# Kernel tuning notes

Measured on AMD Instinct MI355X. Metric: run time of the kernel, lower is better.

## Reference

```python
import jax, jax.numpy as jnp
import numpy as np

B = 1; H = 192; W = 192; DIM = 128; HEADS = 8
WS = 16                      # window_size
OWS = 24                     # overlap_win_size = int(16*0.5)+16
PAD = 4                      # (OWS-WS)//2
C2 = DIM // 2                # per-branch channels
H2 = HEADS // 2              # per-branch heads
HID = 256                    # mlp_ratio * dim
TBL = (WS + OWS - 1) ** 2    # 1521 rel-pos table entries
SCALE = (C2 // H2) ** (-0.5) # head_dim ** -0.5


def layer_norm(x, w, b, eps=1e-5):
    mu = jnp.mean(x, -1, keepdims=True)
    var = jnp.mean((x - mu) ** 2, -1, keepdims=True)
    return (x - mu) * jax.lax.rsqrt(var + eps) * w + b


def window_partition(x, ws):
    b, h, w, c = x.shape
    x = x.reshape(b, h // ws, ws, w // ws, ws, c).transpose(0, 1, 3, 2, 4, 5)
    return x.reshape(-1, ws, ws, c)


def window_reverse(win, ws, h, w):
    b = win.shape[0] // ((h // ws) * (w // ws))
    x = win.reshape(b, h // ws, w // ws, ws, ws, -1).transpose(0, 1, 3, 2, 4, 5)
    return x.reshape(b, h, w, -1)


def _patch_idx(h, w):
    ri = (jnp.arange(h // WS) * WS)[:, None] + jnp.arange(OWS)  # (nwh, OWS)
    ci = (jnp.arange(w // WS) * WS)[:, None] + jnp.arange(OWS)  # (nww, OWS)
    return ri, ci


def unfold_patches(x):
    # x: (b, h, w, c) -> (b*nw, OWS*OWS, c); matches nn.Unfold(OWS, stride=WS, pad=PAD)
    b, h, w, c = x.shape
    xp = jnp.pad(x, ((0, 0), (PAD, PAD), (PAD, PAD), (0, 0)))
    ri, ci = _patch_idx(h, w)
    p = xp[:, ri[:, None, :, None], ci[None, :, None, :], :]  # (b,nwh,nww,OWS,OWS,c)
    return p.reshape(-1, OWS * OWS, c)


def fold_patches(p, b, h, w):
    # inverse of unfold: scatter-add overlapping patches into (b, h+2PAD, w+2PAD, c)
    nwh, nww = h // WS, w // WS
    c = p.shape[-1]
    p = p.reshape(b, nwh, nww, OWS, OWS, c)
    ri, ci = _patch_idx(h, w)
    canvas = jnp.zeros((b, h + 2 * PAD, w + 2 * PAD, c), p.dtype)
    return canvas.at[:, ri[:, None, :, None], ci[None, :, None, :], :].add(p)


def cubic_kernel(x, A=-0.75):
    # PyTorch bicubic (cubic convolution, A=-0.75)
    ax = jnp.abs(x)
    w1 = ((A + 2.0) * ax - (A + 3.0)) * ax * ax + 1.0
    w2 = A * (ax * (ax * (ax - 5.0) + 8.0) - 4.0)
    return jnp.where(ax <= 1.0, w1, jnp.where(ax < 2.0, w2, 0.0))


def resize_matrix(n_out, n_in):
    # dense 1-D bicubic resize matrix, align_corners=False, border-clamped (torch semantics)
    i = jnp.arange(n_out, dtype=jnp.float32)
    src = (i + 0.5) * (float(n_in) / float(n_out)) - 0.5
    fl = jnp.floor(src)
    idx = fl[:, None] + jnp.arange(-1, 3, dtype=jnp.float32)[None, :]  # (n_out, 4)
    wts = cubic_kernel(src[:, None] - idx)
    idx_c = jnp.clip(idx, 0, n_in - 1).astype(jnp.int32)
    M = jnp.zeros((n_out, n_in), jnp.float32)
    return M.at[jnp.arange(n_out)[:, None], idx_c].add(wts)


def cross_attn(xq, xkv, rpi, wq, wkv, rpb):
    b_, nq, d = xq.shape
    n = xkv.shape[1]
    q = (xq @ wq).reshape(b_, nq, H2, -1).transpose(0, 2, 1, 3)
    k, v = jnp.split(xkv @ wkv, 2, axis=-1)
    k = k.reshape(b_, n, H2, -1).transpose(0, 2, 1, 3)
    v = v.reshape(b_, n, H2, -1).transpose(0, 2, 1, 3)
    attn = jnp.einsum('bhqd,bhkd->bhqk', q * SCALE, k)
    bias = rpb[rpi.reshape(-1)].reshape(WS * WS, OWS * OWS, H2)
    bias = bias.transpose(2, 0, 1) if nq < n else bias.transpose(2, 1, 0)
    attn = jax.nn.softmax(attn + bias[None], axis=-1)
    out = jnp.einsum('bhqk,bhkd->bhqd', attn, v)
    return out.transpose(0, 2, 1, 3).reshape(b_, nq, d)


def gsfn(x, h, w, fc1_w, fc1_b, sgn_w, sgn_b, conv_w, conv_b, fc2_w, fc2_b):
    x = x @ fc1_w + fc1_b  # NOTE: source GSFN never applies self.act
    x1, x2 = jnp.split(x, 2, axis=-1)
    Bn, N, Ch = x2.shape
    x2 = layer_norm(x2, sgn_w, sgn_b).transpose(0, 2, 1).reshape(Bn, Ch, h, w)
    x2 = jax.lax.conv_general_dilated(
        x2, conv_w, (1, 1), ((1, 1), (1, 1)),
        feature_group_count=Ch, dimension_numbers=('NCHW', 'OIHW', 'NCHW'))
    x2 = x2 + conv_b[None, :, None, None]
    x2 = x2.reshape(Bn, Ch, N).transpose(0, 2, 1)
    return (x1 * x2) @ fc2_w + fc2_b


def mstb(x_tkn, ln1_w, ln1_b, q1_w, kv1_w, rpb1, q2_w, kv2_w, rpb2,
         proj_w, proj_b, ln2_w, ln2_b, fc1_w, fc1_b, sgn_w, sgn_b,
         conv_w, conv_b, fc2_w, fc2_b, rpi, h, w):
    b, _, c = x_tkn.shape
    short = x_tkn
    x = layer_norm(x_tkn, ln1_w, ln1_b).reshape(b, h, w, c)
    xw = window_partition(x, WS).reshape(-1, WS * WS, c)     # (b*nw, ws*ws, c)
    xa, xb = jnp.split(xw, 2, axis=-1)
    xb_img = window_reverse(xb.reshape(-1, WS, WS, C2), WS, h, w)  # (b,h,w,C2)
    xb_p = unfold_patches(xb_img)                            # (b*nw, OWS*OWS, C2)
    a = cross_attn(xa, xb_p, rpi, q1_w, kv1_w, rpb1) + xa
    bb = cross_attn(xb_p, xa, rpi, q2_w, kv2_w, rpb2) + xb_p
    folded = fold_patches(bb, b, h, w)                       # (b, h+2p, w+2p, C2)
    Mh = resize_matrix(h, h + 2 * PAD)
    Mw = resize_matrix(w, w + 2 * PAD)
    resized = jnp.einsum('oi,bijc,pj->bopc', Mh, folded, Mw)  # bicubic to (h,w)
    xb2 = window_partition(resized, WS).reshape(-1, WS * WS, C2)
    x = jnp.concatenate([a, xb2], -1)
    x = window_reverse(x.reshape(-1, WS, WS, c), WS, h, w).reshape(b, h * w, c)
    x = x @ proj_w + proj_b + short
    x = gsfn(layer_norm(x, ln2_w, ln2_b), h, w, fc1_w, fc1_b,
             sgn_w, sgn_b, conv_w, conv_b, fc2_w, fc2_b) + x
    return x


def setup_inputs() -> dict:
    key = jax.random.key(0)
    ks = jax.random.split(key, 12)
    rn = lambda k, s, sc: jax.random.normal(k, s, jnp.float32) * sc
    return {
        'x_tkn': jax.random.normal(ks[0], (B, H * W, DIM), jnp.float32),
        'ln1_w': jnp.ones((DIM,), jnp.float32), 'ln1_b': jnp.zeros((DIM,), jnp.float32),
        'q1_w': rn(ks[1], (C2, C2), 0.05), 'kv1_w': rn(ks[2], (C2, 2 * C2), 0.05),
        'rpb1': rn(ks[3], (TBL, H2), 0.02),
        'q2_w': rn(ks[4], (C2, C2), 0.05), 'kv2_w': rn(ks[5], (C2, 2 * C2), 0.05),
        'rpb2': rn(ks[6], (TBL, H2), 0.02),
        'proj_w': rn(ks[7], (DIM, DIM), 0.05), 'proj_b': jnp.zeros((DIM,), jnp.float32),
        'ln2_w': jnp.ones((DIM,), jnp.float32), 'ln2_b': jnp.zeros((DIM,), jnp.float32),
        'fc1_w': rn(ks[8], (DIM, HID), 0.05), 'fc1_b': jnp.zeros((HID,), jnp.float32),
        'sgn_w': jnp.ones((HID // 2,), jnp.float32), 'sgn_b': jnp.zeros((HID // 2,), jnp.float32),
        'conv_w': rn(ks[9], (HID // 2, 1, 3, 3), 0.1), 'conv_b': jnp.zeros((HID // 2,), jnp.float32),
        'fc2_w': rn(ks[10], (HID // 2, DIM), 0.05), 'fc2_b': jnp.zeros((DIM,), jnp.float32),
        'rpi': jax.random.randint(ks[11], (WS * WS, OWS * OWS), 0, TBL),
        'h': H, 'w': W,
    }


def reference(x_tkn, ln1_w, ln1_b, q1_w, kv1_w, rpb1, q2_w, kv2_w, rpb2,
              proj_w, proj_b, ln2_w, ln2_b, fc1_w, fc1_b, sgn_w, sgn_b,
              conv_w, conv_b, fc2_w, fc2_b, rpi, h, w):
    return mstb(x_tkn, ln1_w, ln1_b, q1_w, kv1_w, rpb1, q2_w, kv2_w, rpb2,
                proj_w, proj_b, ln2_w, ln2_b, fc1_w, fc1_b, sgn_w, sgn_b,
                conv_w, conv_b, fc2_w, fc2_b, rpi, h, w)
```

## Files before the change

kernel.cpp:

```cpp
#include <hip/hip_runtime.h>
#include <hip/hip_bf16.h>

#define HH 192
#define WW 192
#define NWIN 12
#define WSZ 16
#define OWSZ 24
#define PADK 4
#define NQ1 256
#define NKV1 576
#define C2K 64
#define H2K 4
#define HD 16
#define NTOK (HH*WW)
#define LOG2E 1.4426950408889634f
#define QSCALE (0.25f * LOG2E)

typedef __hip_bfloat16 bf16;
typedef __attribute__((ext_vector_type(8))) short bf16x8;
typedef __attribute__((ext_vector_type(4))) float f32x4;

union B8 { short s[8]; bf16x8 v; unsigned u[4]; };

__device__ __forceinline__ unsigned cvtpk(float lo, float hi)
{
    unsigned r;
    asm("v_cvt_pk_bf16_f32 %0, %1, %2" : "=v"(r) : "v"(lo), "v"(hi));
    return r;
}

__launch_bounds__(256)
__global__ void ln_kernel(const float* __restrict__ in, int is, int io,
                          float* __restrict__ out, int os, int oo,
                          const float* __restrict__ g, const float* __restrict__ b,
                          int M)
{
    int row = blockIdx.x * 4 + (threadIdx.x >> 6);
    if (row >= M) return;
    int lane = threadIdx.x & 63;
    const float* p = in + (size_t)row * is + io;
    float v0 = p[lane * 2], v1 = p[lane * 2 + 1];
    float s = v0 + v1, sq = v0 * v0 + v1 * v1;
#pragma unroll
    for (int o = 32; o > 0; o >>= 1) { s += __shfl_xor(s, o); sq += __shfl_xor(sq, o); }
    float mu  = s * 0.0078125f;
    float var = sq * 0.0078125f - mu * mu;
    float inv = 1.0f / sqrtf(var + 1e-5f);
    float* q = out + (size_t)row * os + oo;
    q[lane * 2]     = (v0 - mu) * inv * g[lane * 2]     + b[lane * 2];
    q[lane * 2 + 1] = (v1 - mu) * inv * g[lane * 2 + 1] + b[lane * 2 + 1];
}

__global__ void wcomb_kernel(const float* __restrict__ q1_w, const float* __restrict__ kv1_w,
                             const float* __restrict__ q2_w, const float* __restrict__ kv2_w,
                             float* __restrict__ W)
{
    int idx = blockIdx.x * 256 + threadIdx.x;
    if (idx >= 128 * 384) return;
    int r = idx / 384, c = idx % 384;
    float v = 0.f;
    if (c < 64)       { if (r < 64)  v = q1_w[r * 64 + c]; }
    else if (c < 192) { if (r >= 64) v = kv1_w[(r - 64) * 128 + (c - 64)]; }
    else if (c < 256) { if (r >= 64) v = q2_w[(r - 64) * 64 + (c - 192)]; }
    else              { if (r < 64)  v = kv2_w[r * 128 + (c - 256)]; }
    W[idx] = v;
}

__global__ void bias1_kernel(const float* __restrict__ rpb1, const int* __restrict__ rpi,
                             float* __restrict__ biasT)
{
    int idx = blockIdx.x * 256 + threadIdx.x;
    if (idx >= H2K * NKV1 * NQ1) return;
    int q = idx & 255;
    int n = (idx >> 8) % NKV1;
    int h = idx / (NKV1 * NQ1);
    biasT[idx] = rpb1[rpi[q * NKV1 + n] * H2K + h] * LOG2E;
}

__global__ void bias2_kernel(const float* __restrict__ rpb2, const int* __restrict__ rpi,
                             float* __restrict__ biasT)
{
    int idx = blockIdx.x * 256 + threadIdx.x;
    if (idx >= H2K * NQ1 * NKV1) return;
    int q = idx % NKV1;
    int k = (idx / NKV1) % NQ1;
    int h = idx / (NKV1 * NQ1);
    biasT[idx] = rpb2[rpi[k * NKV1 + q] * H2K + h] * LOG2E;
}

__launch_bounds__(256)
__global__ void attn1_mfma(const float* __restrict__ qkvA,
                           const float* __restrict__ lnx,
                           const float* __restrict__ biasT,
                           float* __restrict__ xcat)
{
    __shared__ unsigned K_lds[NKV1][12];
    __shared__ unsigned V_lds[NKV1][12];

    const int win = blockIdx.x, h = blockIdx.y;
    const int wi = win / NWIN, wj = win % NWIN;
    const int tid = threadIdx.x;
    const int lane = tid & 63, w = tid >> 6;
    const int g = lane >> 4, qloc = lane & 15;

    for (int n = tid; n < NKV1; n += 256) {
        int rr = wi * WSZ - PADK + n / OWSZ, cc = wj * WSZ - PADK + n % OWSZ;
        bool ib = (rr >= 0 && rr < HH && cc >= 0 && cc < WW);
        unsigned kw[8], vw[8];
        if (ib) {
            const float* kp = qkvA + (size_t)(rr * WW + cc) * 192 + 64 + h * HD;
#pragma unroll
            for (int u = 0; u < 8; u++) {
                kw[u] = cvtpk(kp[2 * u], kp[2 * u + 1]);
                vw[u] = cvtpk(kp[64 + 2 * u], kp[64 + 2 * u + 1]);
            }
        } else {
#pragma unroll
            for (int u = 0; u < 8; u++) { kw[u] = 0; vw[u] = 0; }
        }
        *(uint4*)&K_lds[n][0] = make_uint4(kw[0], kw[1], kw[2], kw[3]);
        *(uint4*)&K_lds[n][4] = make_uint4(kw[4], kw[5], kw[6], kw[7]);
        *(uint4*)&V_lds[n][0] = make_uint4(vw[0], vw[1], vw[2], vw[3]);
        *(uint4*)&V_lds[n][4] = make_uint4(vw[4], vw[5], vw[6], vw[7]);
    }
    __syncthreads();

    const int q0base = blockIdx.z * 128 + w * 32;
    bf16x8 qfrag[2];
#pragma unroll
    for (int qt = 0; qt < 2; qt++) {
        int q = q0base + qt * 16 + qloc;
        int pix = (wi * WSZ + (q >> 4)) * WW + wj * WSZ + (q & 15);
        B8 f;
#pragma unroll
        for (int j = 0; j < 4; j++) f.u[j] = 0;
        if (g < 2) {
            const float* qp = qkvA + (size_t)pix * 192 + h * HD + 8 * g;
#pragma unroll
            for (int j = 0; j < 4; j++)
                f.u[j] = cvtpk(qp[2 * j] * QSCALE, qp[2 * j + 1] * QSCALE);
        }
        qfrag[qt] = f.v;
    }

    f32x4 O[2];
    float lsum[2];
#pragma unroll
    for (int qt = 0; qt < 2; qt++) { O[qt] = (f32x4){0.f, 0.f, 0.f, 0.f}; lsum[qt] = 0.f; }
    const f32x4 zz = {0.f, 0.f, 0.f, 0.f};

    for (int step = 0; step < 18; step++) {
        const int k0 = step * 32;
        bf16x8 kfA, kfB;
        if (g < 2) {
            kfA = *(const bf16x8*)&K_lds[k0 + qloc][4 * g];
            kfB = *(const bf16x8*)&K_lds[k0 + 16 + qloc][4 * g];
        } else {
            B8 zf;
#pragma unroll
            for (int j = 0; j < 4; j++) zf.u[j] = 0;
            kfA = zf.v; kfB = zf.v;
        }
        B8 vf;
#pragma unroll
        for (int j = 0; j < 8; j++) {
            int key = k0 + 4 * g + (j & 3) + ((j >> 2) << 4);
            unsigned word = V_lds[key][qloc >> 1];
            vf.s[j] = (short)((qloc & 1) ? (word >> 16) : (word & 0xffff));
        }

#pragma unroll
        for (int qt = 0; qt < 2; qt++) {
            f32x4 sA = __builtin_amdgcn_mfma_f32_16x16x32_bf16(kfA, qfrag[qt], zz, 0, 0, 0);
            f32x4 sB = __builtin_amdgcn_mfma_f32_16x16x32_bf16(kfB, qfrag[qt], zz, 0, 0, 0);
            int qa = q0base + qt * 16 + qloc;
            const float* bpA = biasT + ((size_t)h * NKV1 + k0 + 4 * g) * NQ1 + qa;
            const float* bpB = bpA + 16 * NQ1;
            float pa[4], pb[4];
            float ls = 0.f;
#pragma unroll
            for (int r = 0; r < 4; r++) {
                pa[r] = exp2f(sA[r] + bpA[(size_t)r * NQ1]);
                pb[r] = exp2f(sB[r] + bpB[(size_t)r * NQ1]);
                ls += pa[r] + pb[r];
            }
            B8 pf;
            pf.u[0] = cvtpk(pa[0], pa[1]);
            pf.u[1] = cvtpk(pa[2], pa[3]);
            pf.u[2] = cvtpk(pb[0], pb[1]);
            pf.u[3] = cvtpk(pb[2], pb[3]);
            lsum[qt] += ls;
            O[qt] = __builtin_amdgcn_mfma_f32_16x16x32_bf16(vf.v, pf.v, O[qt], 0, 0, 0);
        }
    }

#pragma unroll
    for (int qt = 0; qt < 2; qt++) {
        float lt = lsum[qt];
        lt += __shfl_xor(lt, 16);
        lt += __shfl_xor(lt, 32);
        float rl = 1.f / lt;
        int q = q0base + qt * 16 + qloc;
        int pix = (wi * WSZ + (q >> 4)) * WW + wj * WSZ + (q & 15);
        size_t base = (size_t)pix * 128 + h * HD + 4 * g;
#pragma unroll
        for (int r = 0; r < 4; r++)
            xcat[base + r] = O[qt][r] * rl + lnx[base + r];
    }
}

__launch_bounds__(256)
__global__ void attn2_mfma(const float* __restrict__ qkvB,
                           const float* __restrict__ lnx,
                           const float* __restrict__ biasT,
                           float* __restrict__ bb)
{
    __shared__ unsigned K_lds[NQ1][12];
    __shared__ unsigned V_lds[NQ1][12];

    const int win = blockIdx.x, h = blockIdx.y;
    const int wi = win / NWIN, wj = win % NWIN;
    const int tid = threadIdx.x;
    const int lane = tid & 63, w = tid >> 6;
    const int g = lane >> 4, qloc = lane & 15;

    if (tid < NQ1) {
        int n = tid;
        int pix = (wi * WSZ + (n >> 4)) * WW + wj * WSZ + (n & 15);
        const float* kp = qkvB + (size_t)pix * 192 + 64 + h * HD;
        unsigned kw[8], vw[8];
#pragma unroll
        for (int u = 0; u < 8; u++) {
            kw[u] = cvtpk(kp[2 * u], kp[2 * u + 1]);
            vw[u] = cvtpk(kp[64 + 2 * u], kp[64 + 2 * u + 1]);
        }
        *(uint4*)&K_lds[n][0] = make_uint4(kw[0], kw[1], kw[2], kw[3]);
        *(uint4*)&K_lds[n][4] = make_uint4(kw[4], kw[5], kw[6], kw[7]);
        *(uint4*)&V_lds[n][0] = make_uint4(vw[0], vw[1], vw[2], vw[3]);
        *(uint4*)&V_lds[n][4] = make_uint4(vw[4], vw[5], vw[6], vw[7]);
    }
    __syncthreads();

    const int q0base = blockIdx.z * 192 + w * 48;
    bf16x8 qfrag[3];
    bool qin[3];
    int qpix[3];
#pragma unroll
    for (int qt = 0; qt < 3; qt++) {
        int qa = q0base + qt * 16 + qloc;
        int gr = wi * WSZ - PADK + qa / OWSZ, gc = wj * WSZ - PADK + qa % OWSZ;
        bool ib = (gr >= 0 && gr < HH && gc >= 0 && gc < WW);
        qin[qt] = ib;
        qpix[qt] = ib ? gr * WW + gc : 0;
        B8 f;
#pragma unroll
        for (int j = 0; j < 4; j++) f.u[j] = 0;
        if (ib && g < 2) {
            const float* qp = qkvB + (size_t)qpix[qt] * 192 + h * HD + 8 * g;
#pragma unroll
            for (int j = 0; j < 4; j++)
                f.u[j] = cvtpk(qp[2 * j] * QSCALE, qp[2 * j + 1] * QSCALE);
        }
        qfrag[qt] = f.v;
    }

    f32x4 O[3];
    float lsum[3];
#pragma unroll
    for (int qt = 0; qt < 3; qt++) { O[qt] = (f32x4){0.f, 0.f, 0.f, 0.f}; lsum[qt] = 0.f; }
    const f32x4 zz = {0.f, 0.f, 0.f, 0.f};

    for (int step = 0; step < 8; step++) {
        const int k0 = step * 32;
        bf16x8 kfA, kfB;
        if (g < 2) {
            kfA = *(const bf16x8*)&K_lds[k0 + qloc][4 * g];
            kfB = *(const bf16x8*)&K_lds[k0 + 16 + qloc][4 * g];
        } else {
            B8 zf;
#pragma unroll
            for (int j = 0; j < 4; j++) zf.u[j] = 0;
            kfA = zf.v; kfB = zf.v;
        }
        B8 vf;
#pragma unroll
        for (int j = 0; j < 8; j++) {
            int key = k0 + 4 * g + (j & 3) + ((j >> 2) << 4);
            unsigned word = V_lds[key][qloc >> 1];
            vf.s[j] = (short)((qloc & 1) ? (word >> 16) : (word & 0xffff));
        }

#pragma unroll
        for (int qt = 0; qt < 3; qt++) {
            f32x4 sA = __builtin_amdgcn_mfma_f32_16x16x32_bf16(kfA, qfrag[qt], zz, 0, 0, 0);
            f32x4 sB = __builtin_amdgcn_mfma_f32_16x16x32_bf16(kfB, qfrag[qt], zz, 0, 0, 0);
            int qa = q0base + qt * 16 + qloc;
            const float* bpA = biasT + ((size_t)h * NQ1 + k0 + 4 * g) * NKV1 + qa;
            const float* bpB = bpA + 16 * NKV1;
            float pa[4], pb[4];
            float ls = 0.f;
#pragma unroll
            for (int r = 0; r < 4; r++) {
                pa[r] = exp2f(sA[r] + bpA[(size_t)r * NKV1]);
                pb[r] = exp2f(sB[r] + bpB[(size_t)r * NKV1]);
                ls += pa[r] + pb[r];
            }
            B8 pf;
            pf.u[0] = cvtpk(pa[0], pa[1]);
            pf.u[1] = cvtpk(pa[2], pa[3]);
            pf.u[2] = cvtpk(pb[0], pb[1]);
            pf.u[3] = cvtpk(pb[2], pb[3]);
            lsum[qt] += ls;
            O[qt] = __builtin_amdgcn_mfma_f32_16x16x32_bf16(vf.v, pf.v, O[qt], 0, 0, 0);
        }
    }

#pragma unroll
    for (int qt = 0; qt < 3; qt++) {
        float lt = lsum[qt];
        lt += __shfl_xor(lt, 16);
        lt += __shfl_xor(lt, 32);
        float rl = 1.f / lt;
        int qa = q0base + qt * 16 + qloc;
        size_t obase = ((size_t)win * NKV1 + qa) * C2K + h * HD + 4 * g;
        size_t rbase = (size_t)qpix[qt] * 128 + C2K + h * HD + 4 * g;
#pragma unroll
        for (int r = 0; r < 4; r++)
            bb[obase + r] = O[qt][r] * rl + (qin[qt] ? lnx[rbase + r] : 0.f);
    }
}

__global__ void fold_kernel(const float* __restrict__ bb, float* __restrict__ folded)
{
    int idx = blockIdx.x * 256 + threadIdx.x;
    if (idx >= 200 * 200 * 64) return;
    int c = idx & 63;
    int j = (idx >> 6) % 200;
    int i = idx / (64 * 200);
    int ilo = (i > 23) ? ((i - 8) >> 4) : 0;
    int ihi = min(11, i >> 4);
    int jlo = (j > 23) ? ((j - 8) >> 4) : 0;
    int jhi = min(11, j >> 4);
    float s = 0.f;
    for (int wi = ilo; wi <= ihi; wi++)
        for (int wj = jlo; wj <= jhi; wj++) {
            int p = (i - wi * 16) * OWSZ + (j - wj * 16);
            s += bb[((size_t)(wi * NWIN + wj) * NKV1 + p) * C2K + c];
        }
    folded[idx] = s;
}

__device__ __forceinline__ float cubicw(float x)
{
    float ax = fabsf(x);
    const float A = -0.75f;
    if (ax <= 1.f) return ((A + 2.f) * ax - (A + 3.f)) * ax * ax + 1.f;
    if (ax < 2.f)  return A * (ax * (ax * (ax - 5.f) + 8.f) - 4.f);
    return 0.f;
}

__global__ void resize_kernel(const float* __restrict__ folded, float* __restrict__ xcat)
{
    int idx = blockIdx.x * 256 + threadIdx.x;
    if (idx >= HH * WW * C2K) return;
    int c = idx & 63;
    int p = (idx >> 6) % WW;
    int o = idx / (C2K * WW);
    const float ratio = 200.f / 192.f;
    float sr = (o + 0.5f) * ratio - 0.5f;
    float sc = (p + 0.5f) * ratio - 0.5f;
    int fr = (int)floorf(sr), fcc = (int)floorf(sc);
    float wc[4]; int ic[4];
#pragma unroll
    for (int u = 0; u < 4; u++) {
        int jj = fcc - 1 + u;
        wc[u] = cubicw(sc - (float)jj);
        ic[u] = min(max(jj, 0), 199);
    }
    float acc = 0.f;
#pragma unroll
    for (int t = 0; t < 4; t++) {
        int ii = fr - 1 + t;
        float wr = cubicw(sr - (float)ii);
        int ir = min(max(ii, 0), 199);
        const float* rowp = folded + ((size_t)ir * 200) * 64 + c;
        float rs = 0.f;
#pragma unroll
        for (int u = 0; u < 4; u++) rs += wc[u] * rowp[(size_t)ic[u] * 64];
        acc += wr * rs;
    }
    xcat[(size_t)(o * WW + p) * 128 + C2K + c] = acc;
}

template<int NTPW>
__launch_bounds__(256)
__global__ void gemm_mfma(const float* __restrict__ A1, int a1s,
                          const float* __restrict__ A2, int a2s,
                          const float* __restrict__ Wm, int ldb,
                          const float* __restrict__ bias,
                          const float* __restrict__ R, int rs,
                          float* __restrict__ C, int cs)
{
    const int tid = threadIdx.x;
    const int lane = tid & 63, w = tid >> 6;
    const int g = lane >> 4, nl = lane & 15;

    bf16x8 wf[NTPW][4];
#pragma unroll
    for (int t = 0; t < NTPW; t++) {
        int ncol = (w * NTPW + t) * 16 + nl;
#pragma unroll
        for (int ks = 0; ks < 4; ks++) {
            const float* wp = Wm + (size_t)(ks * 32 + 8 * g) * ldb + ncol;
            B8 f;
#pragma unroll
            for (int j = 0; j < 4; j++)
                f.u[j] = cvtpk(wp[(size_t)(2 * j) * ldb], wp[(size_t)(2 * j + 1) * ldb]);
            wf[t][ks] = f.v;
        }
    }

    const f32x4 zz = {0.f, 0.f, 0.f, 0.f};
    for (int it = 0; it < 4; it++) {
        const int row = (blockIdx.x * 4 + it) * 16 + nl;
        bf16x8 xf[4];
        const float* ap = A1 + (size_t)row * a1s + 8 * g;
#pragma unroll
        for (int ks = 0; ks < 4; ks++) {
            float4 v0 = *(const float4*)(ap + ks * 32);
            float4 v1 = *(const float4*)(ap + ks * 32 + 4);
            if (A2) {
                const float* ap2 = A2 + (size_t)row * a2s + 8 * g + ks * 32;
                float4 m0 = *(const float4*)(ap2);
                float4 m1 = *(const float4*)(ap2 + 4);
                v0.x *= m0.x; v0.y *= m0.y; v0.z *= m0.z; v0.w *= m0.w;
                v1.x *= m1.x; v1.y *= m1.y; v1.z *= m1.z; v1.w *= m1.w;
            }
            B8 f;
            f.u[0] = cvtpk(v0.x, v0.y);
            f.u[1] = cvtpk(v0.z, v0.w);
            f.u[2] = cvtpk(v1.x, v1.y);
            f.u[3] = cvtpk(v1.z, v1.w);
            xf[ks] = f.v;
        }

        f32x4 acc[NTPW];
#pragma unroll
        for (int t = 0; t < NTPW; t++) acc[t] = zz;
#pragma unroll
        for (int ks = 0; ks < 4; ks++)
#pragma unroll
            for (int t = 0; t < NTPW; t++)
                acc[t] = __builtin_amdgcn_mfma_f32_16x16x32_bf16(wf[t][ks], xf[ks], acc[t], 0, 0, 0);

#pragma unroll
        for (int t = 0; t < NTPW; t++) {
            const int n0t = (w * NTPW + t) * 16 + 4 * g;
            float4 o;
            o.x = acc[t][0]; o.y = acc[t][1]; o.z = acc[t][2]; o.w = acc[t][3];
            if (bias) {
                float4 bv = *(const float4*)(bias + n0t);
                o.x += bv.x; o.y += bv.y; o.z += bv.z; o.w += bv.w;
            }
            if (R) {
                float4 rv = *(const float4*)(R + (size_t)row * rs + n0t);
                o.x += rv.x; o.y += rv.y; o.z += rv.z; o.w += rv.w;
            }
            *(float4*)(C + (size_t)row * cs + n0t) = o;
        }
    }
}

__global__ void dwconv_kernel(const float* __restrict__ x2n,
                              const float* __restrict__ conv_w,
                              const float* __restrict__ conv_b,
                              float* __restrict__ x2c)
{
    int idx = blockIdx.x * 256 + threadIdx.x;
    if (idx >= NTOK * 128) return;
    int ch = idx & 127, t = idx >> 7;
    int i = t / WW, j = t % WW;
    float acc = conv_b[ch];
#pragma unroll
    for (int a = 0; a < 3; a++) {
        int ii = i + a - 1;
        if (ii < 0 || ii >= HH) continue;
#pragma unroll
        for (int b = 0; b < 3; b++) {
            int jj = j + b - 1;
            if (jj < 0 || jj >= WW) continue;
            acc += conv_w[ch * 9 + a * 3 + b] * x2n[(size_t)(ii * WW + jj) * 256 + ch];
        }
    }
    x2c[(size_t)t * 128 + ch] = acc;
}

extern "C" void kernel_launch(void* const* d_in, const int* in_sizes, int n_in,
                              void* d_out, int out_size, void* d_ws, size_t ws_size,
                              hipStream_t stream)
{
    (void)in_sizes; (void)n_in; (void)out_size; (void)ws_size;
    const float* x_tkn  = (const float*)d_in[0];
    const float* ln1_w  = (const float*)d_in[1];
    const float* ln1_b  = (const float*)d_in[2];
    const float* q1_w   = (const float*)d_in[3];
    const float* kv1_w  = (const float*)d_in[4];
    const float* rpb1   = (const float*)d_in[5];
    const float* q2_w   = (const float*)d_in[6];
    const float* kv2_w  = (const float*)d_in[7];
    const float* rpb2   = (const float*)d_in[8];
    const float* proj_w = (const float*)d_in[9];
    const float* proj_b = (const float*)d_in[10];
    const float* ln2_w  = (const float*)d_in[11];
    const float* ln2_b  = (const float*)d_in[12];
    const float* fc1_w  = (const float*)d_in[13];
    const float* fc1_b  = (const float*)d_in[14];
    const float* sgn_w  = (const float*)d_in[15];
    const float* sgn_b  = (const float*)d_in[16];
    const float* conv_w = (const float*)d_in[17];
    const float* conv_b = (const float*)d_in[18];
    const float* fc2_w  = (const float*)d_in[19];
    const float* fc2_b  = (const float*)d_in[20];
    const int*   rpi    = (const int*)d_in[21];

    float* ws = (float*)d_ws;
    float* lnx    = ws;
    float* xcat   = ws + 4718592;
    float* bbuf   = ws + 9437184;
    float* bias1T = ws + 14745600;
    float* bias2T = ws + 17104896;
    float* wcomb  = ws + 17694720;
    float* qkv    = ws + 17743872;
    float* foldp  = ws + 17743872;
    float* h1     = ws + 14745600;
    float* out    = (float*)d_out;

    ln_kernel<<<NTOK / 4, 256, 0, stream>>>(x_tkn, 128, 0, lnx, 128, 0, ln1_w, ln1_b, NTOK);
    wcomb_kernel<<<(128 * 384 + 255) / 256, 256, 0, stream>>>(q1_w, kv1_w, q2_w, kv2_w, wcomb);
    bias1_kernel<<<(H2K * NKV1 * NQ1) / 256, 256, 0, stream>>>(rpb1, rpi, bias1T);
    bias2_kernel<<<(H2K * NQ1 * NKV1) / 256, 256, 0, stream>>>(rpb2, rpi, bias2T);
    gemm_mfma<3><<<NTOK / 64, 256, 0, stream>>>(lnx, 128, nullptr, 0, wcomb, 384,
                                                nullptr, nullptr, 0, qkv, 192);
    attn1_mfma<<<dim3(144, 4, 2), 256, 0, stream>>>(qkv, lnx, bias1T, xcat);
    gemm_mfma<3><<<NTOK / 64, 256, 0, stream>>>(lnx, 128, nullptr, 0, wcomb + 192, 384,
                                                nullptr, nullptr, 0, qkv, 192);
    attn2_mfma<<<dim3(144, 4, 3), 256, 0, stream>>>(qkv, lnx, bias2T, bbuf);
    fold_kernel<<<(200 * 200 * 64) / 256, 256, 0, stream>>>(bbuf, foldp);
    resize_kernel<<<(HH * WW * C2K) / 256, 256, 0, stream>>>(foldp, xcat);
    gemm_mfma<2><<<NTOK / 64, 256, 0, stream>>>(xcat, 128, nullptr, 0, proj_w, 128,
                                                proj_b, x_tkn, 128, lnx, 128);
    ln_kernel<<<NTOK / 4, 256, 0, stream>>>(lnx, 128, 0, bbuf, 128, 0, ln2_w, ln2_b, NTOK);
    gemm_mfma<4><<<NTOK / 64, 256, 0, stream>>>(bbuf, 128, nullptr, 0, fc1_w, 256,
                                                fc1_b, nullptr, 0, h1, 256);
    ln_kernel<<<NTOK / 4, 256, 0, stream>>>(h1, 256, 128, h1, 256, 128, sgn_w, sgn_b, NTOK);
    dwconv_kernel<<<(NTOK * 128) / 256, 256, 0, stream>>>(h1 + 128, conv_w, conv_b, xcat);
    gemm_mfma<2><<<NTOK / 64, 256, 0, stream>>>(h1, 256, xcat, 128, fc2_w, 128,
                                                fc2_b, lnx, 128, out, 128);
}
```

Baseline: 320.3 us.

## Store QKV in bf16, pre-transpose bf16 weights, and split GEMM rows across grid

The QKV GEMMs now write bf16 output with the attention scale folded into the Q weights, so the attention kernels load K/V/Q fragments directly with vector loads instead of converting fp32 strided data. All GEMM weights are pre-transposed to bf16 so each lane loads a contiguous bf16x8 fragment rather than eight strided fp32 values. Each GEMM block now handles one 16-row tile with a 4x larger grid instead of looping over four tiles, and the LDS row stride shrinks from 12 to 10 words. The costs are extra small transpose kernels, lower-precision intermediate storage of QKV, and weight fragments being reloaded per block.

```diff
diff --git a/kernel.cpp b/kernel.cpp
--- a/kernel.cpp
+++ b/kernel.cpp
@@ -51,19 +51,27 @@
     q[lane * 2 + 1] = (v1 - mu) * inv * g[lane * 2 + 1] + b[lane * 2 + 1];
 }
 
-__global__ void wcomb_kernel(const float* __restrict__ q1_w, const float* __restrict__ kv1_w,
-                             const float* __restrict__ q2_w, const float* __restrict__ kv2_w,
-                             float* __restrict__ W)
-{
-    int idx = blockIdx.x * 256 + threadIdx.x;
-    if (idx >= 128 * 384) return;
-    int r = idx / 384, c = idx % 384;
+__global__ void wcombT_kernel(const float* __restrict__ q1_w, const float* __restrict__ kv1_w,
+                              const float* __restrict__ q2_w, const float* __restrict__ kv2_w,
+                              bf16* __restrict__ WT)
+{
+    int idx = blockIdx.x * 256 + threadIdx.x;
+    if (idx >= 384 * 128) return;
+    int c = idx >> 7, r = idx & 127;
     float v = 0.f;
-    if (c < 64)       { if (r < 64)  v = q1_w[r * 64 + c]; }
+    if (c < 64)       { if (r < 64)  v = q1_w[r * 64 + c] * QSCALE; }
     else if (c < 192) { if (r >= 64) v = kv1_w[(r - 64) * 128 + (c - 64)]; }
-    else if (c < 256) { if (r >= 64) v = q2_w[(r - 64) * 64 + (c - 192)]; }
+    else if (c < 256) { if (r >= 64) v = q2_w[(r - 64) * 64 + (c - 192)] * QSCALE; }
     else              { if (r < 64)  v = kv2_w[r * 128 + (c - 256)]; }
-    W[idx] = v;
+    WT[idx] = __float2bfloat16(v);
+}
+
+__global__ void wtrans_kernel(const float* __restrict__ src, int N, bf16* __restrict__ dst)
+{
+    int idx = blockIdx.x * 256 + threadIdx.x;
+    if (idx >= N * 128) return;
+    int n = idx >> 7, k = idx & 127;
+    dst[idx] = __float2bfloat16(src[(size_t)k * N + n]);
 }
 
 __global__ void bias1_kernel(const float* __restrict__ rpb1, const int* __restrict__ rpi,
@@ -89,13 +97,13 @@
 }
 
 __launch_bounds__(256)
-__global__ void attn1_mfma(const float* __restrict__ qkvA,
+__global__ void attn1_mfma(const unsigned* __restrict__ qkvu,
                            const float* __restrict__ lnx,
                            const float* __restrict__ biasT,
                            float* __restrict__ xcat)
 {
-    __shared__ unsigned K_lds[NKV1][12];
-    __shared__ unsigned V_lds[NKV1][12];
+    __shared__ unsigned K_lds[NKV1][10];
+    __shared__ unsigned V_lds[NKV1][10];
 
     const int win = blockIdx.x, h = blockIdx.y;
     const int wi = win / NWIN, wj = win % NWIN;
@@ -106,22 +114,16 @@
     for (int n = tid; n < NKV1; n += 256) {
         int rr = wi * WSZ - PADK + n / OWSZ, cc = wj * WSZ - PADK + n % OWSZ;
         bool ib = (rr >= 0 && rr < HH && cc >= 0 && cc < WW);
-        unsigned kw[8], vw[8];
+        uint4 k0v = make_uint4(0, 0, 0, 0), k1v = k0v, v0v = k0v, v1v = k0v;
         if (ib) {
-            const float* kp = qkvA + (size_t)(rr * WW + cc) * 192 + 64 + h * HD;
-#pragma unroll
-            for (int u = 0; u < 8; u++) {
-                kw[u] = cvtpk(kp[2 * u], kp[2 * u + 1]);
-                vw[u] = cvtpk(kp[64 + 2 * u], kp[64 + 2 * u + 1]);
-            }
-        } else {
-#pragma unroll
-            for (int u = 0; u < 8; u++) { kw[u] = 0; vw[u] = 0; }
-        }
-        *(uint4*)&K_lds[n][0] = make_uint4(kw[0], kw[1], kw[2], kw[3]);
-        *(uint4*)&K_lds[n][4] = make_uint4(kw[4], kw[5], kw[6], kw[7]);
-        *(uint4*)&V_lds[n][0] = make_uint4(vw[0], vw[1], vw[2], vw[3]);
-        *(uint4*)&V_lds[n][4] = make_uint4(vw[4], vw[5], vw[6], vw[7]);
+            const unsigned* src = qkvu + (size_t)(rr * WW + cc) * 96 + 32 + 8 * h;
+            k0v = *(const uint4*)(src);
+            k1v = *(const uint4*)(src + 4);
+            v0v = *(const uint4*)(src + 32);
+            v1v = *(const uint4*)(src + 36);
+        }
+        *(uint4*)&K_lds[n][0] = k0v; *(uint4*)&K_lds[n][4] = k1v;
+        *(uint4*)&V_lds[n][0] = v0v; *(uint4*)&V_lds[n][4] = v1v;
     }
     __syncthreads();
 
@@ -134,12 +136,8 @@
         B8 f;
 #pragma unroll
         for (int j = 0; j < 4; j++) f.u[j] = 0;
-        if (g < 2) {
-            const float* qp = qkvA + (size_t)pix * 192 + h * HD + 8 * g;
-#pragma unroll
-            for (int j = 0; j < 4; j++)
-                f.u[j] = cvtpk(qp[2 * j] * QSCALE, qp[2 * j + 1] * QSCALE);
-        }
+        if (g < 2)
+            f.v = *(const bf16x8*)(qkvu + (size_t)pix * 96 + 8 * h + 4 * g);
         qfrag[qt] = f.v;
     }
 
@@ -210,13 +208,13 @@
 }
 
 __launch_bounds__(256)
-__global__ void attn2_mfma(const float* __restrict__ qkvB,
+__global__ void attn2_mfma(const unsigned* __restrict__ qkvu,
                            const float* __restrict__ lnx,
                            const float* __restrict__ biasT,
                            float* __restrict__ bb)
 {
-    __shared__ unsigned K_lds[NQ1][12];
-    __shared__ unsigned V_lds[NQ1][12];
+    __shared__ unsigned K_lds[NQ1][10];
+    __shared__ unsigned V_lds[NQ1][10];
 
     const int win = blockIdx.x, h = blockIdx.y;
     const int wi = win / NWIN, wj = win % NWIN;
@@ -224,20 +222,14 @@
     const int lane = tid & 63, w = tid >> 6;
     const int g = lane >> 4, qloc = lane & 15;
 
-    if (tid < NQ1) {
+    {
         int n = tid;
         int pix = (wi * WSZ + (n >> 4)) * WW + wj * WSZ + (n & 15);
-        const float* kp = qkvB + (size_t)pix * 192 + 64 + h * HD;
-        unsigned kw[8], vw[8];
-#pragma unroll
-        for (int u = 0; u < 8; u++) {
-            kw[u] = cvtpk(kp[2 * u], kp[2 * u + 1]);
-            vw[u] = cvtpk(kp[64 + 2 * u], kp[64 + 2 * u + 1]);
-        }
-        *(uint4*)&K_lds[n][0] = make_uint4(kw[0], kw[1], kw[2], kw[3]);
-        *(uint4*)&K_lds[n][4] = make_uint4(kw[4], kw[5], kw[6], kw[7]);
-        *(uint4*)&V_lds[n][0] = make_uint4(vw[0], vw[1], vw[2], vw[3]);
-        *(uint4*)&V_lds[n][4] = make_uint4(vw[4], vw[5], vw[6], vw[7]);
+        const unsigned* src = qkvu + (size_t)pix * 96 + 32 + 8 * h;
+        *(uint4*)&K_lds[n][0] = *(const uint4*)(src);
+        *(uint4*)&K_lds[n][4] = *(const uint4*)(src + 4);
+        *(uint4*)&V_lds[n][0] = *(const uint4*)(src + 32);
+        *(uint4*)&V_lds[n][4] = *(const uint4*)(src + 36);
     }
     __syncthreads();
 
@@ -255,12 +247,8 @@
         B8 f;
 #pragma unroll
         for (int j = 0; j < 4; j++) f.u[j] = 0;
-        if (ib && g < 2) {
-            const float* qp = qkvB + (size_t)qpix[qt] * 192 + h * HD + 8 * g;
-#pragma unroll
-            for (int j = 0; j < 4; j++)
-                f.u[j] = cvtpk(qp[2 * j] * QSCALE, qp[2 * j + 1] * QSCALE);
-        }
+        if (ib && g < 2)
+            f.v = *(const bf16x8*)(qkvu + (size_t)qpix[qt] * 96 + 8 * h + 4 * g);
         qfrag[qt] = f.v;
     }
 
@@ -392,11 +380,11 @@
     xcat[(size_t)(o * WW + p) * 128 + C2K + c] = acc;
 }
 
-template<int NTPW>
+template<int NTPW, bool OBF>
 __launch_bounds__(256)
 __global__ void gemm_mfma(const float* __restrict__ A1, int a1s,
                           const float* __restrict__ A2, int a2s,
-                          const float* __restrict__ Wm, int ldb,
+                          const bf16* __restrict__ WT,
                           const float* __restrict__ bias,
                           const float* __restrict__ R, int rs,
                           float* __restrict__ C, int cs)
@@ -409,53 +397,55 @@
 #pragma unroll
     for (int t = 0; t < NTPW; t++) {
         int ncol = (w * NTPW + t) * 16 + nl;
-#pragma unroll
-        for (int ks = 0; ks < 4; ks++) {
-            const float* wp = Wm + (size_t)(ks * 32 + 8 * g) * ldb + ncol;
-            B8 f;
-#pragma unroll
-            for (int j = 0; j < 4; j++)
-                f.u[j] = cvtpk(wp[(size_t)(2 * j) * ldb], wp[(size_t)(2 * j + 1) * ldb]);
-            wf[t][ks] = f.v;
-        }
+        const bf16* wp = WT + (size_t)ncol * 128;
+#pragma unroll
+        for (int ks = 0; ks < 4; ks++)
+            wf[t][ks] = *(const bf16x8*)(wp + ks * 32 + 8 * g);
     }
 
     const f32x4 zz = {0.f, 0.f, 0.f, 0.f};
-    for (int it = 0; it < 4; it++) {
-        const int row = (blockIdx.x * 4 + it) * 16 + nl;
-        bf16x8 xf[4];
-        const float* ap = A1 + (size_t)row * a1s + 8 * g;
-#pragma unroll
-        for (int ks = 0; ks < 4; ks++) {
-            float4 v0 = *(const float4*)(ap + ks * 32);
-            float4 v1 = *(const float4*)(ap + ks * 32 + 4);
-            if (A2) {
-                const float* ap2 = A2 + (size_t)row * a2s + 8 * g + ks * 32;
-                float4 m0 = *(const float4*)(ap2);
-                float4 m1 = *(const float4*)(ap2 + 4);
-                v0.x *= m0.x; v0.y *= m0.y; v0.z *= m0.z; v0.w *= m0.w;
-                v1.x *= m1.x; v1.y *= m1.y; v1.z *= m1.z; v1.w *= m1.w;
-            }
-            B8 f;
-            f.u[0] = cvtpk(v0.x, v0.y);
-            f.u[1] = cvtpk(v0.z, v0.w);
-            f.u[2] = cvtpk(v1.x, v1.y);
-            f.u[3] = cvtpk(v1.z, v1.w);
-            xf[ks] = f.v;
-        }
-
-        f32x4 acc[NTPW];
-#pragma unroll
-        for (int t = 0; t < NTPW; t++) acc[t] = zz;
-#pragma unroll
-        for (int ks = 0; ks < 4; ks++)
-#pragma unroll
-            for (int t = 0; t < NTPW; t++)
-                acc[t] = __builtin_amdgcn_mfma_f32_16x16x32_bf16(wf[t][ks], xf[ks], acc[t], 0, 0, 0);
-
-#pragma unroll
-        for (int t = 0; t < NTPW; t++) {
-            const int n0t = (w * NTPW + t) * 16 + 4 * g;
+    const int row = (blockIdx.x * 4 + blockIdx.y) * 16 + nl;
+
+    bf16x8 xf[4];
+    const float* ap = A1 + (size_t)row * a1s + 8 * g;
+#pragma unroll
+    for (int ks = 0; ks < 4; ks++) {
+        float4 v0 = *(const float4*)(ap + ks * 32);
+        float4 v1 = *(const float4*)(ap + ks * 32 + 4);
+        if (A2) {
+            const float* ap2 = A2 + (size_t)row * a2s + 8 * g + ks * 32;
+            float4 m0 = *(const float4*)(ap2);
+            float4 m1 = *(const float4*)(ap2 + 4);
+            v0.x *= m0.x; v0.y *= m0.y; v0.z *= m0.z; v0.w *= m0.w;
+            v1.x *= m1.x; v1.y *= m1.y; v1.z *= m1.z; v1.w *= m1.w;
+        }
+        B8 f;
+        f.u[0] = cvtpk(v0.x, v0.y);
+        f.u[1] = cvtpk(v0.z, v0.w);
+        f.u[2] = cvtpk(v1.x, v1.y);
+        f.u[3] = cvtpk(v1.z, v1.w);
+        xf[ks] = f.v;
+    }
+
+    f32x4 acc[NTPW];
+#pragma unroll
+    for (int t = 0; t < NTPW; t++) acc[t] = zz;
+#pragma unroll
+    for (int ks = 0; ks < 4; ks++)
+#pragma unroll
+        for (int t = 0; t < NTPW; t++)
+            acc[t] = __builtin_amdgcn_mfma_f32_16x16x32_bf16(wf[t][ks], xf[ks], acc[t], 0, 0, 0);
+
+#pragma unroll
+    for (int t = 0; t < NTPW; t++) {
+        const int n0t = (w * NTPW + t) * 16 + 4 * g;
+        if (OBF) {
+            unsigned* Cu = (unsigned*)C + (size_t)row * (cs >> 1) + (n0t >> 1);
+            uint2 o;
+            o.x = cvtpk(acc[t][0], acc[t][1]);
+            o.y = cvtpk(acc[t][2], acc[t][3]);
+            *(uint2*)Cu = o;
+        } else {
             float4 o;
             o.x = acc[t][0]; o.y = acc[t][1]; o.z = acc[t][2]; o.w = acc[t][3];
             if (bias) {
@@ -527,33 +517,40 @@
     float* lnx    = ws;
     float* xcat   = ws + 4718592;
     float* bbuf   = ws + 9437184;
+    bf16*  projT  = (bf16*)(ws + 14155776);
+    bf16*  fc1T   = (bf16*)(ws + 14163968);
+    bf16*  fc2T   = (bf16*)(ws + 14180352);
     float* bias1T = ws + 14745600;
     float* bias2T = ws + 17104896;
-    float* wcomb  = ws + 17694720;
-    float* qkv    = ws + 17743872;
-    float* foldp  = ws + 17743872;
+    float* qkv    = ws + 17694720;
+    bf16*  wcombT = (bf16*)(ws + 21233664);
+    float* foldp  = ws + 17694720;
     float* h1     = ws + 14745600;
     float* out    = (float*)d_out;
 
     ln_kernel<<<NTOK / 4, 256, 0, stream>>>(x_tkn, 128, 0, lnx, 128, 0, ln1_w, ln1_b, NTOK);
-    wcomb_kernel<<<(128 * 384 + 255) / 256, 256, 0, stream>>>(q1_w, kv1_w, q2_w, kv2_w, wcomb);
+    wcombT_kernel<<<(384 * 128) / 256, 256, 0, stream>>>(q1_w, kv1_w, q2_w, kv2_w, wcombT);
     bias1_kernel<<<(H2K * NKV1 * NQ1) / 256, 256, 0, stream>>>(rpb1, rpi, bias1T);
     bias2_kernel<<<(H2K * NQ1 * NKV1) / 256, 256, 0, stream>>>(rpb2, rpi, bias2T);
-    gemm_mfma<3><<<NTOK / 64, 256, 0, stream>>>(lnx, 128, nullptr, 0, wcomb, 384,
-                                                nullptr, nullptr, 0, qkv, 192);
-    attn1_mfma<<<dim3(144, 4, 2), 256, 0, stream>>>(qkv, lnx, bias1T, xcat);
-    gemm_mfma<3><<<NTOK / 64, 256, 0, stream>>>(lnx, 128, nullptr, 0, wcomb + 192, 384,
-                                                nullptr, nullptr, 0, qkv, 192);
-    attn2_mfma<<<dim3(144, 4, 3), 256, 0, stream>>>(qkv, lnx, bias2T, bbuf);
+    gemm_mfma<3, true><<<dim3(NTOK / 64, 4), 256, 0, stream>>>(lnx, 128, nullptr, 0, wcombT,
+                                                               nullptr, nullptr, 0, qkv, 192);
+    attn1_mfma<<<dim3(144, 4, 2), 256, 0, stream>>>((const unsigned*)qkv, lnx, bias1T, xcat);
+    gemm_mfma<3, true><<<dim3(NTOK / 64, 4), 256, 0, stream>>>(lnx, 128, nullptr, 0,
+                                                               wcombT + 192 * 128,
+                                                               nullptr, nullptr, 0, qkv, 192);
+    attn2_mfma<<<dim3(144, 4, 3), 256, 0, stream>>>((const unsigned*)qkv, lnx, bias2T, bbuf);
     fold_kernel<<<(200 * 200 * 64) / 256, 256, 0, stream>>>(bbuf, foldp);
+    wtrans_kernel<<<(128 * 128) / 256, 256, 0, stream>>>(proj_w, 128, projT);
+    wtrans_kernel<<<(256 * 128) / 256, 256, 0, stream>>>(fc1_w, 256, fc1T);
+    wtrans_kernel<<<(128 * 128) / 256, 256, 0, stream>>>(fc2_w, 128, fc2T);
     resize_kernel<<<(HH * WW * C2K) / 256, 256, 0, stream>>>(foldp, xcat);
-    gemm_mfma<2><<<NTOK / 64, 256, 0, stream>>>(xcat, 128, nullptr, 0, proj_w, 128,
-                                                proj_b, x_tkn, 128, lnx, 128);
+    gemm_mfma<2, false><<<dim3(NTOK / 64, 4), 256, 0, stream>>>(xcat, 128, nullptr, 0, projT,
+                                                                proj_b, x_tkn, 128, lnx, 128);
     ln_kernel<<<NTOK / 4, 256, 0, stream>>>(lnx, 128, 0, bbuf, 128, 0, ln2_w, ln2_b, NTOK);
-    gemm_mfma<4><<<NTOK / 64, 256, 0, stream>>>(bbuf, 128, nullptr, 0, fc1_w, 256,
-                                                fc1_b, nullptr, 0, h1, 256);
+    gemm_mfma<4, false><<<dim3(NTOK / 64, 4), 256, 0, stream>>>(bbuf, 128, nullptr, 0, fc1T,
+                                                                fc1_b, nullptr, 0, h1, 256);
     ln_kernel<<<NTOK / 4, 256, 0, stream>>>(h1, 256, 128, h1, 256, 128, sgn_w, sgn_b, NTOK);
     dwconv_kernel<<<(NTOK * 128) / 256, 256, 0, stream>>>(h1 + 128, conv_w, conv_b, xcat);
-    gemm_mfma<2><<<NTOK / 64, 256, 0, stream>>>(h1, 256, xcat, 128, fc2_w, 128,
-                                                fc2_b, lnx, 128, out, 128);
-}
+    gemm_mfma<2, false><<<dim3(NTOK / 64, 4), 256, 0, stream>>>(h1, 256, xcat, 128, fc2T,
+                                                                fc2_b, lnx, 128, out, 128);
+}
```

After: 323.3 us. No clear change (+0.9%).
